# Kernel optimization log

Hardware: AMD Instinct MI355X
Metric: run time of the kernel (lower is better)

## Reference

```python
import jax, jax.numpy as jnp
import numpy as np

K = 32
D = 64
N_ITER = 10


def setup_inputs() -> dict:
    key = jax.random.key(0)
    k1, k2 = jax.random.split(key)
    B = 65536
    x = jax.random.normal(k1, (B, D), dtype=jnp.float32)
    c = jnp.zeros((K,), dtype=jnp.float32)
    mu = jax.random.normal(k2, (K, D), dtype=jnp.float32) * 0.1
    A = jnp.tile(jnp.eye(D, dtype=jnp.float32)[None], (K, 1, 1))
    alpha = jnp.float32(0.1)
    return {"x": x, "c": c, "mu": mu, "A": A, "alpha": alpha}


def _grad_phi(x, c, mu, A):
    # Precision matrices Sigma_i^{-1} = A_i^T A_i : (k, d, d)
    P = jnp.einsum('kji,kjl->kil', A, A)
    diff = x[:, None, :] - mu[None, :, :]          # (B, k, d)
    Pd = jnp.einsum('kij,bkj->bki', P, diff)       # Sigma^{-1} (x - mu)
    quad = jnp.einsum('bki,bki->bk', diff, Pd)     # (B, k)
    # Analytic gradient of phi(x) = logsumexp_i(c_i - 0.5 q_i):
    # grad = -sum_i softmax_i(c_i - 0.5 q_i) * Sigma_i^{-1}(x - mu_i)
    w = jax.nn.softmax(c[None, :] - 0.5 * quad, axis=1)  # (B, k)
    return -jnp.einsum('bk,bki->bi', w, Pd)


def reference(x, c, mu, A, alpha):
    def step(x_cur, _):
        x_new = x_cur + alpha * _grad_phi(x_cur, c, mu, A)
        return x_new, None
    x_final, _ = jax.lax.scan(step, x, None, length=N_ITER)
    return x_final
```

## Files before the change

### kernel.cpp

```cpp
#include <hip/hip_runtime.h>
#include <hip/hip_bf16.h>


typedef __attribute__((ext_vector_type(4))) float f32x4;
typedef __attribute__((ext_vector_type(8))) short bf16x8;

#define KC 32
#define NITER 10
#define XROW 72
#define WT_PITCH 40
#define PW_BYTES 3584
#define PSTG 8192

static __device__ __forceinline__ unsigned pk_bf16(float a, float b) {
  __hip_bfloat16 ha = __float2bfloat16(a), hb = __float2bfloat16(b);
  unsigned short ua = *(unsigned short*)&ha, ub = *(unsigned short*)&hb;
  return (unsigned)ua | ((unsigned)ub << 16);
}

static __device__ __forceinline__ float red16(float x) {
#if __has_builtin(__builtin_amdgcn_permlane16_swap)
  int xi = __float_as_int(x);
  auto pr = __builtin_amdgcn_permlane16_swap(xi, xi, false, false);
  return __int_as_float(pr[0]) + __int_as_float(pr[1]);
#else
  int v = __builtin_amdgcn_ds_swizzle(__float_as_int(x), 0x401F);
  return x + __int_as_float(v);
#endif
}
static __device__ __forceinline__ float red32(float x) {
  int xi = __float_as_int(x);
  auto pr = __builtin_amdgcn_permlane32_swap(xi, xi, false, false);
  return __int_as_float(pr[0]) + __int_as_float(pr[1]);
}

static __device__ __forceinline__ void stage16(const void* gsrc, void* ldst) {
  __builtin_amdgcn_global_load_lds(
      (const __attribute__((address_space(1))) unsigned int*)gsrc,
      (__attribute__((address_space(3))) unsigned int*)ldst, 16, 0, 0);
}

__global__ void precompute1(const float* __restrict__ A, const float* __restrict__ mu,
                            const float* __restrict__ c,
                            float* __restrict__ Pmu_g, float* __restrict__ e_g,
                            __hip_bfloat16* __restrict__ Psw) {
  __shared__ float As[64 * 64];
  __shared__ float Pk[64 * 64];
  const int k = blockIdx.x, tid = threadIdx.x;
  const float* Ak = A + k * 4096;
  for (int idx = tid; idx < 1024; idx += 256)
    *(f32x4*)&As[idx * 4] = *(const f32x4*)&Ak[idx * 4];
  __syncthreads();

  const int i = tid >> 2, lg = tid & 3;
  float acc[16] = {};
  for (int j = 0; j < 64; ++j) {
    float ai = As[j * 64 + i];
    const f32x4* row = (const f32x4*)&As[j * 64 + lg * 16];
#pragma unroll
    for (int g = 0; g < 4; ++g) {
      f32x4 v = row[g];
#pragma unroll
      for (int r = 0; r < 4; ++r) acc[g * 4 + r] += ai * v[r];
    }
  }
#pragma unroll
  for (int g = 0; g < 4; ++g)
#pragma unroll
    for (int r = 0; r < 4; ++r) Pk[i * 64 + lg * 16 + g * 4 + r] = acc[g * 4 + r];
  __syncthreads();

  if (tid < 64) {
    float s = 0.f;
    for (int l = 0; l < 64; ++l) s += Pk[l * 64 + tid] * mu[k * 64 + l];
    Pmu_g[k * 64 + tid] = s;
    float v = mu[k * 64 + tid] * s;
#pragma unroll
    for (int off = 1; off < 64; off <<= 1) v += __shfl_xor(v, off, 64);
    if (tid == 0) e_g[k] = c[k] - 0.5f * v;
  }

  unsigned* Psw32 = (unsigned*)(Psw + k * 4096);
  for (int idx2 = tid; idx2 < 2048; idx2 += 256) {
    int idx = idx2 << 1;
    int f = idx >> 9, ln = (idx >> 3) & 63, j = idx & 7;
    int mt = f >> 1, s = f & 1, qq = ln >> 4, l4 = ln & 15;
    int col = mt * 16 + l4, rb = s * 32 + qq * 8 + j;
    Psw32[idx2] = pk_bf16(Pk[rb * 64 + col], Pk[(rb + 1) * 64 + col]);
  }
}

__global__ void precompute2(const float* __restrict__ Pmu_g,
                            __hip_bfloat16* __restrict__ PmuA,
                            __hip_bfloat16* __restrict__ PmuB) {
  const int tid = threadIdx.x;
  for (int idx = tid; idx < 2048; idx += 256) {
    int f = idx >> 9, lane = (idx >> 3) & 63, j = idx & 7;
    int mtc = f >> 1, s = f & 1, qq = lane >> 4, l4 = lane & 15;
    PmuA[idx] = __float2bfloat16(Pmu_g[(mtc * 16 + l4) * 64 + s * 32 + qq * 8 + j]);
  }
  for (int idx = tid; idx < 2048; idx += 256) {
    int f = idx >> 9, lane = (idx >> 3) & 63, j = idx & 7;
    int qq = lane >> 4, l4 = lane & 15;
    PmuB[idx] = __float2bfloat16(Pmu_g[(qq * 8 + j) * 64 + f * 16 + l4]);
  }
}

__launch_bounds__(256, 4)
__global__ void denoise_main(const float* __restrict__ x_in,
                             const float* __restrict__ e_g,
                             const float* __restrict__ alpha_g,
                             const __hip_bfloat16* __restrict__ Psw,
                             const __hip_bfloat16* __restrict__ PmuA,
                             const __hip_bfloat16* __restrict__ PmuB,
                             float* __restrict__ out) {
  __shared__ __attribute__((aligned(16))) char scratch[4 * PW_BYTES + 2 * PSTG];

  const int tid = threadIdx.x;
  const int wave = tid >> 6, lane = tid & 63;
  const int q = lane >> 4, l4 = lane & 15;
  const int base_pt = blockIdx.x * 64 + wave * 16;
  const float alpha = alpha_g[0];

  char* pw = scratch + wave * PW_BYTES;
  __hip_bfloat16* xsw = (__hip_bfloat16*)pw;
  float* pmxw = (float*)pw;
  __hip_bfloat16* wtw = (__hip_bfloat16*)(pw + 2304);
  char* pstg = scratch + 4 * PW_BYTES;

  const char* PswB = (const char*)Psw;
  const bf16x8* PmuAF = (const bf16x8*)PmuA;
  const bf16x8* PmuBF = (const bf16x8*)PmuB;

  f32x4 xm[4];
#pragma unroll
  for (int mt = 0; mt < 4; ++mt)
    xm[mt] = *(const f32x4*)&x_in[(base_pt + l4) * 64 + mt * 16 + q * 4];

  f32x4 ev[2];
#pragma unroll
  for (int mtc = 0; mtc < 2; ++mtc) ev[mtc] = *(const f32x4*)&e_g[mtc * 16 + q * 4];

  const f32x4 Z4 = {0.f, 0.f, 0.f, 0.f};
  const int f0 = 2 * wave, f1 = 2 * wave + 1;

#pragma unroll 1
  for (int it = 0; it < NITER; ++it) {
    stage16(PswB + f0 * 1024 + lane * 16, pstg + f0 * 1024);
    stage16(PswB + f1 * 1024 + lane * 16, pstg + f1 * 1024);

#pragma unroll
    for (int mt = 0; mt < 4; ++mt) {
      uint2 v;
      v.x = pk_bf16(xm[mt][0], xm[mt][1]);
      v.y = pk_bf16(xm[mt][2], xm[mt][3]);
      *(uint2*)&xsw[l4 * XROW + mt * 16 + q * 4] = v;
    }

    bf16x8 bx[2];
#pragma unroll
    for (int s = 0; s < 2; ++s)
      bx[s] = *(const bf16x8*)&xsw[l4 * XROW + s * 32 + q * 8];

    f32x4 pmx[2];
#pragma unroll
    for (int mtc = 0; mtc < 2; ++mtc) {
      f32x4 acc = Z4;
#pragma unroll
      for (int s = 0; s < 2; ++s) {
        bf16x8 a = PmuAF[(mtc * 2 + s) * 64 + lane];
        acc = __builtin_amdgcn_mfma_f32_16x16x32_bf16(a, bx[s], acc, 0, 0, 0);
      }
      pmx[mtc] = acc;
    }
#pragma unroll
    for (int mtc = 0; mtc < 2; ++mtc)
#pragma unroll
      for (int r = 0; r < 4; ++r)
        pmxw[(mtc * 16 + q * 4 + r) * 16 + l4] = pmx[mtc][r] + ev[mtc][r];

    f32x4 accY[4];
#pragma unroll
    for (int mt = 0; mt < 4; ++mt) accY[mt] = Z4;
    float lsum = 0.f;

    __syncthreads();

#pragma unroll 2
    for (int k = 0; k < KC; ++k) {
      const int cur = k & 1;
      if (k < KC - 1) {
        const char* ps = PswB + (k + 1) * PSTG;
        char* pd = pstg + (cur ^ 1) * PSTG;
        stage16(ps + f0 * 1024 + lane * 16, pd + f0 * 1024);
        stage16(ps + f1 * 1024 + lane * 16, pd + f1 * 1024);
      }

      const char* pc = pstg + cur * PSTG;
      bf16x8 ap[4][2];
#pragma unroll
      for (int mt = 0; mt < 4; ++mt)
#pragma unroll
        for (int s = 0; s < 2; ++s)
          ap[mt][s] = *(const bf16x8*)(pc + (mt * 2 + s) * 1024 + lane * 16);

      f32x4 y[4];
#pragma unroll
      for (int mt = 0; mt < 4; ++mt) {
        f32x4 acc = Z4;
        acc = __builtin_amdgcn_mfma_f32_16x16x32_bf16(ap[mt][0], bx[0], acc, 0, 0, 0);
        acc = __builtin_amdgcn_mfma_f32_16x16x32_bf16(ap[mt][1], bx[1], acc, 0, 0, 0);
        y[mt] = acc;
      }

      f32x4 d = xm[0] * y[0];
#pragma unroll
      for (int mt = 1; mt < 4; ++mt) d += xm[mt] * y[mt];
      const float xy = red32(red16((d[0] + d[1]) + (d[2] + d[3])));

      const float pk = pmxw[k * 16 + l4];
      const float w = __expf(pk - 0.5f * xy);
      lsum += w;
      if (q == 0) wtw[l4 * WT_PITCH + k] = __float2bfloat16(w);
#pragma unroll
      for (int mt = 0; mt < 4; ++mt) accY[mt] += w * y[mt];

      __syncthreads();
    }

    bf16x8 wtf = *(const bf16x8*)&wtw[l4 * WT_PITCH + q * 8];
    f32x4 pacc[4];
#pragma unroll
    for (int mt = 0; mt < 4; ++mt)
      pacc[mt] = __builtin_amdgcn_mfma_f32_16x16x32_bf16(PmuBF[mt * 64 + lane], wtf, Z4, 0, 0, 0);

    const float cc = alpha / lsum;
#pragma unroll
    for (int mt = 0; mt < 4; ++mt) xm[mt] += cc * (pacc[mt] - accY[mt]);
  }

#pragma unroll
  for (int mt = 0; mt < 4; ++mt)
    *(f32x4*)&out[(base_pt + l4) * 64 + mt * 16 + q * 4] = xm[mt];
}

extern "C" void kernel_launch(void* const* d_in, const int* in_sizes, int n_in,
                              void* d_out, int out_size, void* d_ws, size_t ws_size,
                              hipStream_t stream) {
  (void)in_sizes; (void)n_in; (void)out_size; (void)ws_size;
  const float* x = (const float*)d_in[0];
  const float* c = (const float*)d_in[1];
  const float* mu = (const float*)d_in[2];
  const float* A = (const float*)d_in[3];
  const float* alpha = (const float*)d_in[4];
  float* out = (float*)d_out;

  char* ws = (char*)d_ws;
  float* Pmu_g = (float*)(ws);
  float* e_g = (float*)(ws + 8192);
  __hip_bfloat16* PmuA = (__hip_bfloat16*)(ws + 8448);
  __hip_bfloat16* PmuB = (__hip_bfloat16*)(ws + 12544);
  __hip_bfloat16* Psw = (__hip_bfloat16*)(ws + 16640);

  precompute1<<<32, 256, 0, stream>>>(A, mu, c, Pmu_g, e_g, Psw);
  precompute2<<<1, 256, 0, stream>>>(Pmu_g, PmuA, PmuB);
  denoise_main<<<1024, 256, 0, stream>>>(x, e_g, alpha, Psw, PmuA, PmuB, out);
}
```

Measured before the change: 307.9 us.

## Switch to 32x32 MFMA tiles with register-prefetched P and no block syncs

```diff
diff --git a/kernel.cpp b/kernel.cpp
--- a/kernel.cpp
+++ b/kernel.cpp
@@ -3,14 +3,14 @@
 
 
 typedef __attribute__((ext_vector_type(4))) float f32x4;
+typedef __attribute__((ext_vector_type(16))) float f32x16;
 typedef __attribute__((ext_vector_type(8))) short bf16x8;
 
 #define KC 32
 #define NITER 10
 #define XROW 72
 #define WT_PITCH 40
-#define PW_BYTES 3584
-#define PSTG 8192
+#define PW_BYTES 7296
 
 static __device__ __forceinline__ unsigned pk_bf16(float a, float b) {
   __hip_bfloat16 ha = __float2bfloat16(a), hb = __float2bfloat16(b);
@@ -18,230 +18,207 @@
   return (unsigned)ua | ((unsigned)ub << 16);
 }
 
-static __device__ __forceinline__ float red16(float x) {
-#if __has_builtin(__builtin_amdgcn_permlane16_swap)
-  int xi = __float_as_int(x);
-  auto pr = __builtin_amdgcn_permlane16_swap(xi, xi, false, false);
-  return __int_as_float(pr[0]) + __int_as_float(pr[1]);
-#else
-  int v = __builtin_amdgcn_ds_swizzle(__float_as_int(x), 0x401F);
-  return x + __int_as_float(v);
-#endif
-}
 static __device__ __forceinline__ float red32(float x) {
   int xi = __float_as_int(x);
   auto pr = __builtin_amdgcn_permlane32_swap(xi, xi, false, false);
   return __int_as_float(pr[0]) + __int_as_float(pr[1]);
 }
 
-static __device__ __forceinline__ void stage16(const void* gsrc, void* ldst) {
-  __builtin_amdgcn_global_load_lds(
-      (const __attribute__((address_space(1))) unsigned int*)gsrc,
-      (__attribute__((address_space(3))) unsigned int*)ldst, 16, 0, 0);
-}
-
 __global__ void precompute1(const float* __restrict__ A, const float* __restrict__ mu,
-                            const float* __restrict__ c,
-                            float* __restrict__ Pmu_g, float* __restrict__ e_g,
+                            float* __restrict__ ep_g,
+                            __hip_bfloat16* __restrict__ PmuA,
+                            __hip_bfloat16* __restrict__ PmuB,
                             __hip_bfloat16* __restrict__ Psw) {
   __shared__ float As[64 * 64];
-  __shared__ float Pk[64 * 64];
-  const int k = blockIdx.x, tid = threadIdx.x;
+  __shared__ float Ps[64 * 16];
+  __shared__ float Pmu_s[16];
+  const int k = blockIdx.x >> 2, st = blockIdx.x & 3, tid = threadIdx.x;
   const float* Ak = A + k * 4096;
   for (int idx = tid; idx < 1024; idx += 256)
     *(f32x4*)&As[idx * 4] = *(const f32x4*)&Ak[idx * 4];
   __syncthreads();
 
   const int i = tid >> 2, lg = tid & 3;
-  float acc[16] = {};
+  f32x4 acc = {0.f, 0.f, 0.f, 0.f};
   for (int j = 0; j < 64; ++j) {
     float ai = As[j * 64 + i];
-    const f32x4* row = (const f32x4*)&As[j * 64 + lg * 16];
-#pragma unroll
-    for (int g = 0; g < 4; ++g) {
-      f32x4 v = row[g];
-#pragma unroll
-      for (int r = 0; r < 4; ++r) acc[g * 4 + r] += ai * v[r];
-    }
-  }
-#pragma unroll
-  for (int g = 0; g < 4; ++g)
-#pragma unroll
-    for (int r = 0; r < 4; ++r) Pk[i * 64 + lg * 16 + g * 4 + r] = acc[g * 4 + r];
+    f32x4 v = *(const f32x4*)&As[j * 64 + st * 16 + lg * 4];
+    acc += ai * v;
+  }
+  *(f32x4*)&Ps[i * 16 + lg * 4] = acc;
   __syncthreads();
 
   if (tid < 64) {
+    const int c = tid & 15, lh = tid >> 4;
     float s = 0.f;
-    for (int l = 0; l < 64; ++l) s += Pk[l * 64 + tid] * mu[k * 64 + l];
-    Pmu_g[k * 64 + tid] = s;
-    float v = mu[k * 64 + tid] * s;
-#pragma unroll
-    for (int off = 1; off < 64; off <<= 1) v += __shfl_xor(v, off, 64);
-    if (tid == 0) e_g[k] = c[k] - 0.5f * v;
+#pragma unroll
+    for (int ll = 0; ll < 16; ++ll) s += Ps[(lh * 16 + ll) * 16 + c] * mu[k * 64 + lh * 16 + ll];
+    s += __shfl_xor(s, 16, 64);
+    s += __shfl_xor(s, 32, 64);
+    if (lh == 0) Pmu_s[c] = s;
+  }
+  __syncthreads();
+
+  if (tid == 0) {
+    float v = 0.f;
+#pragma unroll
+    for (int c2 = 0; c2 < 16; ++c2) v += mu[k * 64 + st * 16 + c2] * Pmu_s[c2];
+    ep_g[k * 4 + st] = v;
+  }
+
+  if (tid < 16) {
+    const int dl = tid;
+    __hip_bfloat16 pv = __float2bfloat16(Pmu_s[dl]);
+    PmuA[st * 512 + (dl >> 3) * 256 + k * 8 + (dl & 7)] = pv;
+    PmuB[((st >> 1) * 2 + (k >> 4)) * 512 + (((k >> 3) & 1) * 32 + (st & 1) * 16 + dl) * 8 +
+         (k & 7)] = pv;
   }
 
   unsigned* Psw32 = (unsigned*)(Psw + k * 4096);
-  for (int idx2 = tid; idx2 < 2048; idx2 += 256) {
-    int idx = idx2 << 1;
-    int f = idx >> 9, ln = (idx >> 3) & 63, j = idx & 7;
-    int mt = f >> 1, s = f & 1, qq = ln >> 4, l4 = ln & 15;
-    int col = mt * 16 + l4, rb = s * 32 + qq * 8 + j;
-    Psw32[idx2] = pk_bf16(Pk[rb * 64 + col], Pk[(rb + 1) * 64 + col]);
-  }
-}
-
-__global__ void precompute2(const float* __restrict__ Pmu_g,
-                            __hip_bfloat16* __restrict__ PmuA,
-                            __hip_bfloat16* __restrict__ PmuB) {
-  const int tid = threadIdx.x;
-  for (int idx = tid; idx < 2048; idx += 256) {
-    int f = idx >> 9, lane = (idx >> 3) & 63, j = idx & 7;
-    int mtc = f >> 1, s = f & 1, qq = lane >> 4, l4 = lane & 15;
-    PmuA[idx] = __float2bfloat16(Pmu_g[(mtc * 16 + l4) * 64 + s * 32 + qq * 8 + j]);
-  }
-  for (int idx = tid; idx < 2048; idx += 256) {
-    int f = idx >> 9, lane = (idx >> 3) & 63, j = idx & 7;
-    int qq = lane >> 4, l4 = lane & 15;
-    PmuB[idx] = __float2bfloat16(Pmu_g[(qq * 8 + j) * 64 + f * 16 + l4]);
-  }
-}
-
-__launch_bounds__(256, 4)
+  for (int idx2 = tid; idx2 < 512; idx2 += 256) {
+    int mt = idx2 >> 8, rem = idx2 & 255;
+    int l = rem >> 2, jj = rem & 3;
+    int row = mt * 32 + (l & 31), cl = (l >> 5) * 8 + 2 * jj;
+    Psw32[(mt * 4 + st) * 256 + rem] = pk_bf16(Ps[row * 16 + cl], Ps[row * 16 + cl + 1]);
+  }
+}
+
+__launch_bounds__(256, 2)
 __global__ void denoise_main(const float* __restrict__ x_in,
-                             const float* __restrict__ e_g,
+                             const float* __restrict__ c_g,
+                             const float* __restrict__ ep_g,
                              const float* __restrict__ alpha_g,
                              const __hip_bfloat16* __restrict__ Psw,
                              const __hip_bfloat16* __restrict__ PmuA,
                              const __hip_bfloat16* __restrict__ PmuB,
                              float* __restrict__ out) {
-  __shared__ __attribute__((aligned(16))) char scratch[4 * PW_BYTES + 2 * PSTG];
+  __shared__ __attribute__((aligned(16))) char scratch[4 * PW_BYTES];
 
   const int tid = threadIdx.x;
   const int wave = tid >> 6, lane = tid & 63;
-  const int q = lane >> 4, l4 = lane & 15;
-  const int base_pt = blockIdx.x * 64 + wave * 16;
+  const int pt = lane & 31, h = lane >> 5;
+  const int base_pt = blockIdx.x * 128 + wave * 32;
   const float alpha = alpha_g[0];
 
   char* pw = scratch + wave * PW_BYTES;
   __hip_bfloat16* xsw = (__hip_bfloat16*)pw;
   float* pmxw = (float*)pw;
-  __hip_bfloat16* wtw = (__hip_bfloat16*)(pw + 2304);
-  char* pstg = scratch + 4 * PW_BYTES;
-
-  const char* PswB = (const char*)Psw;
+  __hip_bfloat16* wtw = (__hip_bfloat16*)(pw + 4608);
+  float* eww = (float*)(pw + 7168);
+
+  const bf16x8* PswF = (const bf16x8*)Psw;
   const bf16x8* PmuAF = (const bf16x8*)PmuA;
   const bf16x8* PmuBF = (const bf16x8*)PmuB;
 
-  f32x4 xm[4];
-#pragma unroll
-  for (int mt = 0; mt < 4; ++mt)
-    xm[mt] = *(const f32x4*)&x_in[(base_pt + l4) * 64 + mt * 16 + q * 4];
-
-  f32x4 ev[2];
-#pragma unroll
-  for (int mtc = 0; mtc < 2; ++mtc) ev[mtc] = *(const f32x4*)&e_g[mtc * 16 + q * 4];
-
-  const f32x4 Z4 = {0.f, 0.f, 0.f, 0.f};
-  const int f0 = 2 * wave, f1 = 2 * wave + 1;
+  if (lane < 32) {
+    const f32x4 ep = *(const f32x4*)&ep_g[lane * 4];
+    eww[lane] = c_g[lane] - 0.5f * ((ep[0] + ep[1]) + (ep[2] + ep[3]));
+  }
+
+  f32x4 xm[2][4];
+#pragma unroll
+  for (int t = 0; t < 2; ++t)
+#pragma unroll
+    for (int rq = 0; rq < 4; ++rq)
+      xm[t][rq] = *(const f32x4*)&x_in[(base_pt + pt) * 64 + t * 32 + 8 * rq + 4 * h];
+
+  const f32x16 Z16 = {0.f, 0.f, 0.f, 0.f, 0.f, 0.f, 0.f, 0.f,
+                      0.f, 0.f, 0.f, 0.f, 0.f, 0.f, 0.f, 0.f};
 
 #pragma unroll 1
   for (int it = 0; it < NITER; ++it) {
-    stage16(PswB + f0 * 1024 + lane * 16, pstg + f0 * 1024);
-    stage16(PswB + f1 * 1024 + lane * 16, pstg + f1 * 1024);
-
-#pragma unroll
-    for (int mt = 0; mt < 4; ++mt) {
-      uint2 v;
-      v.x = pk_bf16(xm[mt][0], xm[mt][1]);
-      v.y = pk_bf16(xm[mt][2], xm[mt][3]);
-      *(uint2*)&xsw[l4 * XROW + mt * 16 + q * 4] = v;
+#pragma unroll
+    for (int t = 0; t < 2; ++t)
+#pragma unroll
+      for (int rq = 0; rq < 4; ++rq) {
+        uint2 v;
+        v.x = pk_bf16(xm[t][rq][0], xm[t][rq][1]);
+        v.y = pk_bf16(xm[t][rq][2], xm[t][rq][3]);
+        *(uint2*)&xsw[pt * XROW + t * 32 + 8 * rq + 4 * h] = v;
+      }
+
+    bf16x8 bx[4];
+#pragma unroll
+    for (int c = 0; c < 4; ++c)
+      bx[c] = *(const bf16x8*)&xsw[pt * XROW + c * 16 + h * 8];
+
+    bf16x8 ap[2][8];
+#pragma unroll
+    for (int f = 0; f < 8; ++f) ap[0][f] = PswF[f * 64 + lane];
+
+    f32x16 pmx = Z16;
+#pragma unroll
+    for (int c = 0; c < 4; ++c)
+      pmx = __builtin_amdgcn_mfma_f32_32x32x16_bf16(PmuAF[c * 64 + lane], bx[c], pmx, 0, 0, 0);
+#pragma unroll
+    for (int r = 0; r < 16; ++r) {
+      const int cl = (r & 3) + 8 * (r >> 2) + 4 * h;
+      pmxw[cl * 32 + pt] = pmx[r] + eww[cl];
     }
 
-    bf16x8 bx[2];
-#pragma unroll
-    for (int s = 0; s < 2; ++s)
-      bx[s] = *(const bf16x8*)&xsw[l4 * XROW + s * 32 + q * 8];
-
-    f32x4 pmx[2];
-#pragma unroll
-    for (int mtc = 0; mtc < 2; ++mtc) {
-      f32x4 acc = Z4;
-#pragma unroll
-      for (int s = 0; s < 2; ++s) {
-        bf16x8 a = PmuAF[(mtc * 2 + s) * 64 + lane];
-        acc = __builtin_amdgcn_mfma_f32_16x16x32_bf16(a, bx[s], acc, 0, 0, 0);
-      }
-      pmx[mtc] = acc;
-    }
-#pragma unroll
-    for (int mtc = 0; mtc < 2; ++mtc)
-#pragma unroll
-      for (int r = 0; r < 4; ++r)
-        pmxw[(mtc * 16 + q * 4 + r) * 16 + l4] = pmx[mtc][r] + ev[mtc][r];
-
-    f32x4 accY[4];
-#pragma unroll
-    for (int mt = 0; mt < 4; ++mt) accY[mt] = Z4;
+    f32x16 accY0 = Z16, accY1 = Z16;
     float lsum = 0.f;
-
-    __syncthreads();
 
 #pragma unroll 2
     for (int k = 0; k < KC; ++k) {
-      const int cur = k & 1;
-      if (k < KC - 1) {
-        const char* ps = PswB + (k + 1) * PSTG;
-        char* pd = pstg + (cur ^ 1) * PSTG;
-        stage16(ps + f0 * 1024 + lane * 16, pd + f0 * 1024);
-        stage16(ps + f1 * 1024 + lane * 16, pd + f1 * 1024);
+      const int cur = k & 1, nxt = cur ^ 1;
+      const int kn = (k + 1) & (KC - 1);
+#pragma unroll
+      for (int f = 0; f < 8; ++f) ap[nxt][f] = PswF[kn * 512 + f * 64 + lane];
+
+      f32x16 y0, y1;
+      y0 = __builtin_amdgcn_mfma_f32_32x32x16_bf16(ap[cur][0], bx[0], Z16, 0, 0, 0);
+      y1 = __builtin_amdgcn_mfma_f32_32x32x16_bf16(ap[cur][4], bx[0], Z16, 0, 0, 0);
+      y0 = __builtin_amdgcn_mfma_f32_32x32x16_bf16(ap[cur][1], bx[1], y0, 0, 0, 0);
+      y1 = __builtin_amdgcn_mfma_f32_32x32x16_bf16(ap[cur][5], bx[1], y1, 0, 0, 0);
+      y0 = __builtin_amdgcn_mfma_f32_32x32x16_bf16(ap[cur][2], bx[2], y0, 0, 0, 0);
+      y1 = __builtin_amdgcn_mfma_f32_32x32x16_bf16(ap[cur][6], bx[2], y1, 0, 0, 0);
+      y0 = __builtin_amdgcn_mfma_f32_32x32x16_bf16(ap[cur][3], bx[3], y0, 0, 0, 0);
+      y1 = __builtin_amdgcn_mfma_f32_32x32x16_bf16(ap[cur][7], bx[3], y1, 0, 0, 0);
+
+      f32x4 d = {0.f, 0.f, 0.f, 0.f};
+#pragma unroll
+      for (int rq = 0; rq < 4; ++rq) {
+        f32x4 yq0 = {y0[4 * rq], y0[4 * rq + 1], y0[4 * rq + 2], y0[4 * rq + 3]};
+        f32x4 yq1 = {y1[4 * rq], y1[4 * rq + 1], y1[4 * rq + 2], y1[4 * rq + 3]};
+        d += xm[0][rq] * yq0;
+        d += xm[1][rq] * yq1;
       }
-
-      const char* pc = pstg + cur * PSTG;
-      bf16x8 ap[4][2];
-#pragma unroll
-      for (int mt = 0; mt < 4; ++mt)
-#pragma unroll
-        for (int s = 0; s < 2; ++s)
-          ap[mt][s] = *(const bf16x8*)(pc + (mt * 2 + s) * 1024 + lane * 16);
-
-      f32x4 y[4];
-#pragma unroll
-      for (int mt = 0; mt < 4; ++mt) {
-        f32x4 acc = Z4;
-        acc = __builtin_amdgcn_mfma_f32_16x16x32_bf16(ap[mt][0], bx[0], acc, 0, 0, 0);
-        acc = __builtin_amdgcn_mfma_f32_16x16x32_bf16(ap[mt][1], bx[1], acc, 0, 0, 0);
-        y[mt] = acc;
-      }
-
-      f32x4 d = xm[0] * y[0];
-#pragma unroll
-      for (int mt = 1; mt < 4; ++mt) d += xm[mt] * y[mt];
-      const float xy = red32(red16((d[0] + d[1]) + (d[2] + d[3])));
-
-      const float pk = pmxw[k * 16 + l4];
+      const float xy = red32((d[0] + d[1]) + (d[2] + d[3]));
+
+      const float pk = pmxw[k * 32 + pt];
       const float w = __expf(pk - 0.5f * xy);
       lsum += w;
-      if (q == 0) wtw[l4 * WT_PITCH + k] = __float2bfloat16(w);
-#pragma unroll
-      for (int mt = 0; mt < 4; ++mt) accY[mt] += w * y[mt];
-
-      __syncthreads();
+      if (lane < 32) wtw[pt * WT_PITCH + k] = __float2bfloat16(w);
+      accY0 += y0 * w;
+      accY1 += y1 * w;
     }
 
-    bf16x8 wtf = *(const bf16x8*)&wtw[l4 * WT_PITCH + q * 8];
-    f32x4 pacc[4];
-#pragma unroll
-    for (int mt = 0; mt < 4; ++mt)
-      pacc[mt] = __builtin_amdgcn_mfma_f32_16x16x32_bf16(PmuBF[mt * 64 + lane], wtf, Z4, 0, 0, 0);
+    bf16x8 wtf0 = *(const bf16x8*)&wtw[pt * WT_PITCH + h * 8];
+    bf16x8 wtf1 = *(const bf16x8*)&wtw[pt * WT_PITCH + 16 + h * 8];
+    f32x16 pacc0, pacc1;
+    pacc0 = __builtin_amdgcn_mfma_f32_32x32x16_bf16(PmuBF[0 * 64 + lane], wtf0, Z16, 0, 0, 0);
+    pacc1 = __builtin_amdgcn_mfma_f32_32x32x16_bf16(PmuBF[2 * 64 + lane], wtf0, Z16, 0, 0, 0);
+    pacc0 = __builtin_amdgcn_mfma_f32_32x32x16_bf16(PmuBF[1 * 64 + lane], wtf1, pacc0, 0, 0, 0);
+    pacc1 = __builtin_amdgcn_mfma_f32_32x32x16_bf16(PmuBF[3 * 64 + lane], wtf1, pacc1, 0, 0, 0);
 
     const float cc = alpha / lsum;
 #pragma unroll
-    for (int mt = 0; mt < 4; ++mt) xm[mt] += cc * (pacc[mt] - accY[mt]);
-  }
-
-#pragma unroll
-  for (int mt = 0; mt < 4; ++mt)
-    *(f32x4*)&out[(base_pt + l4) * 64 + mt * 16 + q * 4] = xm[mt];
+    for (int rq = 0; rq < 4; ++rq) {
+      f32x4 p0 = {pacc0[4 * rq], pacc0[4 * rq + 1], pacc0[4 * rq + 2], pacc0[4 * rq + 3]};
+      f32x4 a0 = {accY0[4 * rq], accY0[4 * rq + 1], accY0[4 * rq + 2], accY0[4 * rq + 3]};
+      xm[0][rq] += cc * (p0 - a0);
+      f32x4 p1 = {pacc1[4 * rq], pacc1[4 * rq + 1], pacc1[4 * rq + 2], pacc1[4 * rq + 3]};
+      f32x4 a1 = {accY1[4 * rq], accY1[4 * rq + 1], accY1[4 * rq + 2], accY1[4 * rq + 3]};
+      xm[1][rq] += cc * (p1 - a1);
+    }
+  }
+
+#pragma unroll
+  for (int t = 0; t < 2; ++t)
+#pragma unroll
+    for (int rq = 0; rq < 4; ++rq)
+      *(f32x4*)&out[(base_pt + pt) * 64 + t * 32 + 8 * rq + 4 * h] = xm[t][rq];
 }
 
 extern "C" void kernel_launch(void* const* d_in, const int* in_sizes, int n_in,
@@ -256,13 +233,11 @@
   float* out = (float*)d_out;
 
   char* ws = (char*)d_ws;
-  float* Pmu_g = (float*)(ws);
-  float* e_g = (float*)(ws + 8192);
-  __hip_bfloat16* PmuA = (__hip_bfloat16*)(ws + 8448);
-  __hip_bfloat16* PmuB = (__hip_bfloat16*)(ws + 12544);
-  __hip_bfloat16* Psw = (__hip_bfloat16*)(ws + 16640);
-
-  precompute1<<<32, 256, 0, stream>>>(A, mu, c, Pmu_g, e_g, Psw);
-  precompute2<<<1, 256, 0, stream>>>(Pmu_g, PmuA, PmuB);
-  denoise_main<<<1024, 256, 0, stream>>>(x, e_g, alpha, Psw, PmuA, PmuB, out);
-}
+  float* ep_g = (float*)ws;
+  __hip_bfloat16* PmuA = (__hip_bfloat16*)(ws + 1024);
+  __hip_bfloat16* PmuB = (__hip_bfloat16*)(ws + 5120);
+  __hip_bfloat16* Psw = (__hip_bfloat16*)(ws + 9216);
+
+  precompute1<<<128, 256, 0, stream>>>(A, mu, ep_g, PmuA, PmuB, Psw);
+  denoise_main<<<512, 256, 0, stream>>>(x, c, ep_g, alpha, Psw, PmuA, PmuB, out);
+}
```

Measured after the change: 262.2 us. 1.17x faster.
